# Optimization experiments

Hardware: AMD Instinct MI355X
Metric: run time of the kernel (lower is better)

The kernel has to match this reference:

```python
import jax, jax.numpy as jnp
import numpy as np

C, U, V, D, B = 5, 6144, 6144, 64, 4096  # classes, users, items, feat dim, batch pairs


def setup_inputs() -> dict:
    key = jax.random.key(0)
    ks = jax.random.split(key, 16)
    s = 1.0 / np.sqrt(D)
    adj = (jax.random.uniform(ks[0], (C, U, V)) < 0.01).astype(jnp.float32)
    return {
        "u": jax.random.randint(ks[1], (B,), 0, U),
        "v": jax.random.randint(ks[2], (B,), 0, V),
        "u_emb": jax.random.normal(ks[3], (U, D), jnp.float32) * 0.1,
        "v_emb": jax.random.normal(ks[4], (V, D), jnp.float32) * 0.1,
        "W1u": jax.random.normal(ks[5], (C, D, D), jnp.float32) * s,
        "b1u": jnp.zeros((C, D), jnp.float32),
        "W1v": jax.random.normal(ks[6], (C, D, D), jnp.float32) * s,
        "b1v": jnp.zeros((C, D), jnp.float32),
        "W2u": jax.random.normal(ks[7], (C, D, D), jnp.float32) * s,
        "b2u": jnp.zeros((C, D), jnp.float32),
        "W2v": jax.random.normal(ks[8], (C, D, D), jnp.float32) * s,
        "b2v": jnp.zeros((C, D), jnp.float32),
        "Q": jax.random.normal(ks[9], (C, D, D), jnp.float32) * s,
        "adj": adj,
    }


def reference(u, v, u_emb, v_emb, W1u, b1u, W1v, b1v, W2u, b2u, W2v, b2v, Q, adj):
    # ---- layer 1: per-class graph convolution, summed over rating classes ----
    # user codes aggregate item features through adj_c; item codes through adj_c^T
    msg_v = jnp.einsum("vd,cde->cve", v_emb, W1v)            # [C,V,D]
    h_u = jax.nn.relu(jnp.einsum("cuv,cve->ue", adj, msg_v) + b1v.sum(0))  # [U,D]
    msg_u = jnp.einsum("ud,cde->cue", u_emb, W1u)            # [C,U,D]
    h_v = jax.nn.relu(jnp.einsum("cuv,cue->ve", adj, msg_u) + b1u.sum(0))  # [V,D]
    # ---- layer 2 ----
    z_u = jnp.einsum("cuv,cve->ue", adj, jnp.einsum("vd,cde->cve", h_v, W2u)) + b2u.sum(0)
    z_v = jnp.einsum("cuv,cue->ve", adj, jnp.einsum("ud,cde->cue", h_u, W2v)) + b2v.sum(0)
    # ---- bilinear decoder over batch of (user, item) pairs ----
    zu = z_u[u]                                              # [B,D] gather
    zv = z_v[v]                                              # [B,D] gather
    logits = jnp.einsum("bd,cde,be->bc", zu, Q, zv)          # [B,C] per-class rating logits
    return logits
```

## Files before the change

kernel.cpp:

```cpp
#include <hip/hip_runtime.h>

#define NC   5
#define NU   6144
#define NV   6144
#define ND   64
#define NB   4096
#define CAP  128
#define NW   192

__device__ __forceinline__ unsigned int spread4(unsigned int x) {
  x &= 0xFFu;
  x = (x | (x << 12)) & 0x000F000Fu;
  x = (x | (x << 6))  & 0x03030303u;
  x = (x | (x << 3))  & 0x11111111u;
  return x;
}

__global__ __launch_bounds__(256) void k_bitmask(
    const float* __restrict__ adj,
    unsigned int* __restrict__ rowmask,
    unsigned int* __restrict__ colmask) {
  __shared__ unsigned int rowwords[64][8];
  const int b = blockIdx.x;
  const int c  = b / 2304;
  const int rem = b - c * 2304;
  const int tu = rem / 24;
  const int tv = rem - tu * 24;
  const int wave = threadIdx.x >> 6;
  const int lane = threadIdx.x & 63;

  for (int rr = 0; rr < 16; ++rr) {
    const int r = wave * 16 + rr;
    const float4* src = (const float4*)(adj +
        ((size_t)(c * NU + tu * 64 + r) * NV + tv * 256));
    const float4 a = src[lane];
    const unsigned long long b0 = __ballot(a.x != 0.0f);
    const unsigned long long b1 = __ballot(a.y != 0.0f);
    const unsigned long long b2 = __ballot(a.z != 0.0f);
    const unsigned long long b3 = __ballot(a.w != 0.0f);
    if (lane < 8) {
      const unsigned int e0 = spread4((unsigned int)(b0 >> (lane * 8)));
      const unsigned int e1 = spread4((unsigned int)(b1 >> (lane * 8)));
      const unsigned int e2 = spread4((unsigned int)(b2 >> (lane * 8)));
      const unsigned int e3 = spread4((unsigned int)(b3 >> (lane * 8)));
      rowwords[r][lane] = e0 | (e1 << 1) | (e2 << 2) | (e3 << 3);
    }
  }
  __syncthreads();

  {
    const int r2 = threadIdx.x >> 2;
    const int k  = threadIdx.x & 3;
    uint2 w;
    w.x = rowwords[r2][k * 2 + 0];
    w.y = rowwords[r2][k * 2 + 1];
    *(uint2*)(rowmask + (size_t)(c * NU + tu * 64 + r2) * NW + tv * 8 + k * 2) = w;
  }

  {
    const int j = threadIdx.x;
    const int w = j >> 5, bit = j & 31;
    unsigned int w0 = 0, w1 = 0;
    #pragma unroll
    for (int r = 0; r < 32; ++r) {
      w0 |= ((rowwords[r][w]      >> bit) & 1u) << r;
      w1 |= ((rowwords[r + 32][w] >> bit) & 1u) << r;
    }
    uint2 ww; ww.x = w0; ww.y = w1;
    *(uint2*)(colmask + (size_t)(c * NV + tv * 256 + j) * NW + tu * 2) = ww;
  }
}

__global__ __launch_bounds__(256) void k_expand(
    const unsigned int* __restrict__ mask,
    int* __restrict__ cnt,
    unsigned short* __restrict__ idx) {
  const int wave = threadIdx.x >> 6;
  const int lane = threadIdx.x & 63;
  const int R = blockIdx.x * 4 + wave;
  const unsigned int* mrow = mask + (size_t)R * NW;
  const unsigned int w0 = mrow[lane];
  const unsigned int w1 = mrow[lane + 64];
  const unsigned int w2 = mrow[lane + 128];
  const int t0 = __popc(w0), t1 = __popc(w1), t2 = __popc(w2);
  int p0 = t0, p1 = t1, p2 = t2;
  #pragma unroll
  for (int d = 1; d < 64; d <<= 1) {
    const int y0 = __shfl_up(p0, d, 64);
    const int y1 = __shfl_up(p1, d, 64);
    const int y2 = __shfl_up(p2, d, 64);
    if (lane >= d) { p0 += y0; p1 += y1; p2 += y2; }
  }
  const int T0 = __shfl(p0, 63, 64);
  const int T1 = __shfl(p1, 63, 64);
  const int T2 = __shfl(p2, 63, 64);
  if (lane == 0) cnt[R] = T0 + T1 + T2;
  unsigned short* orow = idx + (size_t)R * CAP;
  int e0 = p0 - t0;
  int e1 = T0 + p1 - t1;
  int e2 = T0 + T1 + p2 - t2;
  unsigned int m;
  m = w0;
  while (m) { int bb = __ffs(m) - 1; if (e0 < CAP) orow[e0] = (unsigned short)(lane * 32 + bb); ++e0; m &= m - 1; }
  m = w1;
  while (m) { int bb = __ffs(m) - 1; if (e1 < CAP) orow[e1] = (unsigned short)((lane + 64) * 32 + bb); ++e1; m &= m - 1; }
  m = w2;
  while (m) { int bb = __ffs(m) - 1; if (e2 < CAP) orow[e2] = (unsigned short)((lane + 128) * 32 + bb); ++e2; m &= m - 1; }
}

__global__ __launch_bounds__(256) void k_emb_transform(
    const float* __restrict__ emb,
    const float* __restrict__ W,
    float* __restrict__ out,
    int N) {
  const int c    = blockIdx.y;
  const int lane = threadIdx.x & 63;
  const int wave = threadIdx.x >> 6;
  const float* Wc = W + c * 64 * 64;
  float w[64];
  #pragma unroll
  for (int d = 0; d < 64; ++d) w[d] = Wc[d * 64 + lane];
  const int row0 = blockIdx.x * 64 + wave;
  for (int i = 0; i < 16; ++i) {
    const int r = row0 + i * 4;
    const float* er = emb + (size_t)r * 64;
    float acc = 0.0f;
    #pragma unroll
    for (int d = 0; d < 64; ++d) acc = fmaf(er[d], w[d], acc);
    out[((size_t)c * N + r) * 64 + lane] = acc;
  }
}

__global__ __launch_bounds__(256) void k_spmm(
    const int* __restrict__ cnt,
    const unsigned short* __restrict__ idx,
    const float* __restrict__ msg,
    const float* __restrict__ bias,
    float* __restrict__ out,
    int M, int N, int do_relu) {
  __shared__ float4 red4[4][16];
  const int r    = blockIdx.x;
  const int wave = threadIdx.x >> 6;
  const int lane = threadIdx.x & 63;
  const int g    = lane >> 4;
  const int e16  = lane & 15;
  float4 acc = make_float4(0.f, 0.f, 0.f, 0.f);
  for (int c = wave; c < NC; c += 4) {
    int n = cnt[c * M + r];
    n = n > CAP ? CAP : n;
    const unsigned short* l = idx + (size_t)(c * M + r) * CAP;
    const float4* msgc = (const float4*)msg + (size_t)c * N * 16;
    for (int i = 0; i < n; i += 4) {
      const int ig = i + g;
      if (ig < n) {
        const float4 x = msgc[(int)l[ig] * 16 + e16];
        acc.x += x.x; acc.y += x.y; acc.z += x.z; acc.w += x.w;
      }
    }
  }
  #pragma unroll
  for (int off = 16; off < 64; off <<= 1) {
    acc.x += __shfl_xor(acc.x, off, 64);
    acc.y += __shfl_xor(acc.y, off, 64);
    acc.z += __shfl_xor(acc.z, off, 64);
    acc.w += __shfl_xor(acc.w, off, 64);
  }
  if (lane < 16) red4[wave][e16] = acc;
  __syncthreads();
  if (threadIdx.x < 16) {
    const int e = threadIdx.x;
    float4 s = red4[0][e];
    #pragma unroll
    for (int w = 1; w < 4; ++w) {
      s.x += red4[w][e].x; s.y += red4[w][e].y;
      s.z += red4[w][e].z; s.w += red4[w][e].w;
    }
    #pragma unroll
    for (int c = 0; c < NC; ++c) {
      const float4 bb = ((const float4*)bias)[c * 16 + e];
      s.x += bb.x; s.y += bb.y; s.z += bb.z; s.w += bb.w;
    }
    if (do_relu) {
      s.x = fmaxf(s.x, 0.f); s.y = fmaxf(s.y, 0.f);
      s.z = fmaxf(s.z, 0.f); s.w = fmaxf(s.w, 0.f);
    }
    ((float4*)out)[(size_t)r * 16 + e] = s;
  }
}

__global__ __launch_bounds__(256) void k_decoder(
    const int* __restrict__ uu, const int* __restrict__ vv,
    const float* __restrict__ z_u, const float* __restrict__ z_v,
    const float* __restrict__ Q,
    float* __restrict__ out) {
  const int lane = threadIdx.x & 63;
  const int wave = threadIdx.x >> 6;
  const int b = blockIdx.x * 4 + wave;
  const int ub = uu[b];
  const int vb = vv[b];
  const float zve = z_v[(size_t)vb * 64 + lane];
  const float* zu = z_u + (size_t)ub * 64;
  #pragma unroll
  for (int c = 0; c < NC; ++c) {
    const float* Qc = Q + c * 64 * 64;
    float t = 0.0f;
    #pragma unroll
    for (int d = 0; d < 64; ++d) t = fmaf(zu[d], Qc[d * 64 + lane], t);
    float p = t * zve;
    #pragma unroll
    for (int off = 32; off > 0; off >>= 1) p += __shfl_xor(p, off, 64);
    if (lane == 0) out[(size_t)b * NC + c] = p;
  }
}

extern "C" void kernel_launch(void* const* d_in, const int* in_sizes, int n_in,
                              void* d_out, int out_size, void* d_ws, size_t ws_size,
                              hipStream_t stream) {
  const int*   u     = (const int*)d_in[0];
  const int*   v     = (const int*)d_in[1];
  const float* u_emb = (const float*)d_in[2];
  const float* v_emb = (const float*)d_in[3];
  const float* W1u   = (const float*)d_in[4];
  const float* b1u   = (const float*)d_in[5];
  const float* W1v   = (const float*)d_in[6];
  const float* b1v   = (const float*)d_in[7];
  const float* W2u   = (const float*)d_in[8];
  const float* b2u   = (const float*)d_in[9];
  const float* W2v   = (const float*)d_in[10];
  const float* b2v   = (const float*)d_in[11];
  const float* Q     = (const float*)d_in[12];
  const float* adj   = (const float*)d_in[13];
  float* out = (float*)d_out;

  char* ws = (char*)d_ws;
  int* csr_cnt = (int*)ws;
  int* csc_cnt = csr_cnt + NC * NU;
  unsigned short* csr_idx = (unsigned short*)(ws + 245760);
  unsigned short* csc_idx = (unsigned short*)(ws + 245760 + 7864320);
  char* maskbase = ws + 245760 + 2 * 7864320;
  unsigned int* rowmask = (unsigned int*)maskbase;
  unsigned int* colmask = (unsigned int*)(maskbase + 23592960);
  float* msgA = (float*)maskbase;
  float* msgB = (float*)(maskbase + 7864320);
  float* h_u  = (float*)(maskbase + 15728640);
  float* h_v  = (float*)(maskbase + 17301504);
  float* z_u  = (float*)(maskbase + 18874368);
  float* z_v  = (float*)(maskbase + 20447232);

  k_bitmask<<<5 * 96 * 24, 256, 0, stream>>>(adj, rowmask, colmask);
  k_expand<<<NC * NU / 4, 256, 0, stream>>>(rowmask, csr_cnt, csr_idx);
  k_expand<<<NC * NV / 4, 256, 0, stream>>>(colmask, csc_cnt, csc_idx);

  const dim3 gT(NU / 64, NC);
  k_emb_transform<<<gT, 256, 0, stream>>>(v_emb, W1v, msgA, NV);
  k_emb_transform<<<gT, 256, 0, stream>>>(u_emb, W1u, msgB, NU);
  k_spmm<<<NU, 256, 0, stream>>>(csr_cnt, csr_idx, msgA, b1v, h_u, NU, NV, 1);
  k_spmm<<<NV, 256, 0, stream>>>(csc_cnt, csc_idx, msgB, b1u, h_v, NV, NU, 1);
  k_emb_transform<<<gT, 256, 0, stream>>>(h_v, W2u, msgA, NV);
  k_emb_transform<<<gT, 256, 0, stream>>>(h_u, W2v, msgB, NU);
  k_spmm<<<NU, 256, 0, stream>>>(csr_cnt, csr_idx, msgA, b2u, z_u, NU, NV, 0);
  k_spmm<<<NV, 256, 0, stream>>>(csc_cnt, csc_idx, msgB, b2v, z_v, NV, NU, 0);
  k_decoder<<<NB / 4, 256, 0, stream>>>(u, v, z_u, z_v, Q, out);
}
```

Baseline: 1.388 ms.

## Reorder graph conv to aggregate-then-transform and batch adjacency loads in bitmask

The per-class graph convolution is reassociated: raw embeddings are gathered and summed per class through the CSR/CSC lists first, and the 64x64 weight transform is applied afterwards in a fused 5-class GEMM kernel that also adds the bias and ReLU. This removes the per-class message tables and lets the gather read a single compact embedding table that is more cache-friendly. The gather gets four independent accumulators for more loads in flight. The bitmask kernel now issues all 16 row loads before the ballots to raise memory-level parallelism. The cost is an extra aggregate buffer round-trip and a different floating-point summation order.

```diff
diff --git a/kernel.cpp b/kernel.cpp
--- a/kernel.cpp
+++ b/kernel.cpp
@@ -29,21 +29,26 @@
   const int wave = threadIdx.x >> 6;
   const int lane = threadIdx.x & 63;
 
+  float4 av[16];
+  {
+    const float* base = adj +
+        ((size_t)(c * NU + tu * 64 + wave * 16) * NV + tv * 256);
+    #pragma unroll
+    for (int rr = 0; rr < 16; ++rr)
+      av[rr] = ((const float4*)(base + (size_t)rr * NV))[lane];
+  }
+  #pragma unroll
   for (int rr = 0; rr < 16; ++rr) {
-    const int r = wave * 16 + rr;
-    const float4* src = (const float4*)(adj +
-        ((size_t)(c * NU + tu * 64 + r) * NV + tv * 256));
-    const float4 a = src[lane];
-    const unsigned long long b0 = __ballot(a.x != 0.0f);
-    const unsigned long long b1 = __ballot(a.y != 0.0f);
-    const unsigned long long b2 = __ballot(a.z != 0.0f);
-    const unsigned long long b3 = __ballot(a.w != 0.0f);
+    const unsigned long long b0 = __ballot(av[rr].x != 0.0f);
+    const unsigned long long b1 = __ballot(av[rr].y != 0.0f);
+    const unsigned long long b2 = __ballot(av[rr].z != 0.0f);
+    const unsigned long long b3 = __ballot(av[rr].w != 0.0f);
     if (lane < 8) {
       const unsigned int e0 = spread4((unsigned int)(b0 >> (lane * 8)));
       const unsigned int e1 = spread4((unsigned int)(b1 >> (lane * 8)));
       const unsigned int e2 = spread4((unsigned int)(b2 >> (lane * 8)));
       const unsigned int e3 = spread4((unsigned int)(b3 >> (lane * 8)));
-      rowwords[r][lane] = e0 | (e1 << 1) | (e2 << 2) | (e3 << 3);
+      rowwords[wave * 16 + rr][lane] = e0 | (e1 << 1) | (e2 << 2) | (e3 << 3);
     }
   }
   __syncthreads();
@@ -108,83 +113,93 @@
   while (m) { int bb = __ffs(m) - 1; if (e2 < CAP) orow[e2] = (unsigned short)((lane + 128) * 32 + bb); ++e2; m &= m - 1; }
 }
 
-__global__ __launch_bounds__(256) void k_emb_transform(
-    const float* __restrict__ emb,
-    const float* __restrict__ W,
-    float* __restrict__ out,
-    int N) {
-  const int c    = blockIdx.y;
-  const int lane = threadIdx.x & 63;
-  const int wave = threadIdx.x >> 6;
-  const float* Wc = W + c * 64 * 64;
-  float w[64];
-  #pragma unroll
-  for (int d = 0; d < 64; ++d) w[d] = Wc[d * 64 + lane];
-  const int row0 = blockIdx.x * 64 + wave;
-  for (int i = 0; i < 16; ++i) {
-    const int r = row0 + i * 4;
-    const float* er = emb + (size_t)r * 64;
-    float acc = 0.0f;
-    #pragma unroll
-    for (int d = 0; d < 64; ++d) acc = fmaf(er[d], w[d], acc);
-    out[((size_t)c * N + r) * 64 + lane] = acc;
-  }
-}
-
-__global__ __launch_bounds__(256) void k_spmm(
+__global__ __launch_bounds__(256) void k_gather(
     const int* __restrict__ cnt,
     const unsigned short* __restrict__ idx,
-    const float* __restrict__ msg,
+    const float* __restrict__ table,
+    float* __restrict__ agg) {
+  __shared__ float4 red4[4][16];
+  const int wave = threadIdx.x >> 6;
+  const int lane = threadIdx.x & 63;
+  const int R = blockIdx.x * 4 + wave;
+  const int g    = lane >> 4;
+  const int e16  = lane & 15;
+  int n = cnt[R];
+  n = n > CAP ? CAP : n;
+  const unsigned short* l = idx + (size_t)R * CAP;
+  const float4* tab = (const float4*)table;
+  float4 a0 = make_float4(0.f,0.f,0.f,0.f), a1 = a0, a2 = a0, a3 = a0;
+  int i = 0;
+  for (; i + 16 <= n; i += 16) {
+    const int j0 = l[i + g], j1 = l[i + 4 + g];
+    const int j2 = l[i + 8 + g], j3 = l[i + 12 + g];
+    const float4 x0 = tab[j0 * 16 + e16];
+    const float4 x1 = tab[j1 * 16 + e16];
+    const float4 x2 = tab[j2 * 16 + e16];
+    const float4 x3 = tab[j3 * 16 + e16];
+    a0.x += x0.x; a0.y += x0.y; a0.z += x0.z; a0.w += x0.w;
+    a1.x += x1.x; a1.y += x1.y; a1.z += x1.z; a1.w += x1.w;
+    a2.x += x2.x; a2.y += x2.y; a2.z += x2.z; a2.w += x2.w;
+    a3.x += x3.x; a3.y += x3.y; a3.z += x3.z; a3.w += x3.w;
+  }
+  for (; i + 4 <= n; i += 4) {
+    const float4 x = tab[(int)l[i + g] * 16 + e16];
+    a0.x += x.x; a0.y += x.y; a0.z += x.z; a0.w += x.w;
+  }
+  if (i + g < n) {
+    const float4 x = tab[(int)l[i + g] * 16 + e16];
+    a1.x += x.x; a1.y += x.y; a1.z += x.z; a1.w += x.w;
+  }
+  a0.x += a1.x + a2.x + a3.x;
+  a0.y += a1.y + a2.y + a3.y;
+  a0.z += a1.z + a2.z + a3.z;
+  a0.w += a1.w + a2.w + a3.w;
+  #pragma unroll
+  for (int off = 16; off < 64; off <<= 1) {
+    a0.x += __shfl_xor(a0.x, off, 64);
+    a0.y += __shfl_xor(a0.y, off, 64);
+    a0.z += __shfl_xor(a0.z, off, 64);
+    a0.w += __shfl_xor(a0.w, off, 64);
+  }
+  if (g == 0) red4[wave][e16] = a0;
+  __syncthreads();
+  if (g == 0) ((float4*)agg)[(size_t)R * 16 + e16] = red4[wave][e16];
+}
+
+__global__ __launch_bounds__(256) void k_gemm5(
+    const float* __restrict__ agg,
+    const float* __restrict__ W,
     const float* __restrict__ bias,
     float* __restrict__ out,
-    int M, int N, int do_relu) {
-  __shared__ float4 red4[4][16];
-  const int r    = blockIdx.x;
-  const int wave = threadIdx.x >> 6;
-  const int lane = threadIdx.x & 63;
-  const int g    = lane >> 4;
-  const int e16  = lane & 15;
-  float4 acc = make_float4(0.f, 0.f, 0.f, 0.f);
-  for (int c = wave; c < NC; c += 4) {
-    int n = cnt[c * M + r];
-    n = n > CAP ? CAP : n;
-    const unsigned short* l = idx + (size_t)(c * M + r) * CAP;
-    const float4* msgc = (const float4*)msg + (size_t)c * N * 16;
-    for (int i = 0; i < n; i += 4) {
-      const int ig = i + g;
-      if (ig < n) {
-        const float4 x = msgc[(int)l[ig] * 16 + e16];
-        acc.x += x.x; acc.y += x.y; acc.z += x.z; acc.w += x.w;
+    int M, int do_relu) {
+  const int lane = threadIdx.x & 63;
+  const int wave = threadIdx.x >> 6;
+  const int r0 = blockIdx.x * 16 + wave * 4;
+  float bs = 0.0f;
+  #pragma unroll
+  for (int c = 0; c < NC; ++c) bs += bias[c * 64 + lane];
+  float acc[4] = {bs, bs, bs, bs};
+  for (int c = 0; c < NC; ++c) {
+    float w[64];
+    #pragma unroll
+    for (int d = 0; d < 64; ++d) w[d] = W[c * 4096 + d * 64 + lane];
+    #pragma unroll
+    for (int r = 0; r < 4; ++r) {
+      const float4* ar = (const float4*)(agg + ((size_t)c * M + r0 + r) * 64);
+      #pragma unroll
+      for (int d4 = 0; d4 < 16; ++d4) {
+        const float4 a = ar[d4];
+        acc[r] = fmaf(a.x, w[d4 * 4 + 0], acc[r]);
+        acc[r] = fmaf(a.y, w[d4 * 4 + 1], acc[r]);
+        acc[r] = fmaf(a.z, w[d4 * 4 + 2], acc[r]);
+        acc[r] = fmaf(a.w, w[d4 * 4 + 3], acc[r]);
       }
     }
   }
   #pragma unroll
-  for (int off = 16; off < 64; off <<= 1) {
-    acc.x += __shfl_xor(acc.x, off, 64);
-    acc.y += __shfl_xor(acc.y, off, 64);
-    acc.z += __shfl_xor(acc.z, off, 64);
-    acc.w += __shfl_xor(acc.w, off, 64);
-  }
-  if (lane < 16) red4[wave][e16] = acc;
-  __syncthreads();
-  if (threadIdx.x < 16) {
-    const int e = threadIdx.x;
-    float4 s = red4[0][e];
-    #pragma unroll
-    for (int w = 1; w < 4; ++w) {
-      s.x += red4[w][e].x; s.y += red4[w][e].y;
-      s.z += red4[w][e].z; s.w += red4[w][e].w;
-    }
-    #pragma unroll
-    for (int c = 0; c < NC; ++c) {
-      const float4 bb = ((const float4*)bias)[c * 16 + e];
-      s.x += bb.x; s.y += bb.y; s.z += bb.z; s.w += bb.w;
-    }
-    if (do_relu) {
-      s.x = fmaxf(s.x, 0.f); s.y = fmaxf(s.y, 0.f);
-      s.z = fmaxf(s.z, 0.f); s.w = fmaxf(s.w, 0.f);
-    }
-    ((float4*)out)[(size_t)r * 16 + e] = s;
+  for (int r = 0; r < 4; ++r) {
+    const float x = do_relu ? fmaxf(acc[r], 0.0f) : acc[r];
+    out[(size_t)(r0 + r) * 64 + lane] = x;
   }
 }
 
@@ -240,8 +255,8 @@
   char* maskbase = ws + 245760 + 2 * 7864320;
   unsigned int* rowmask = (unsigned int*)maskbase;
   unsigned int* colmask = (unsigned int*)(maskbase + 23592960);
-  float* msgA = (float*)maskbase;
-  float* msgB = (float*)(maskbase + 7864320);
+  float* aggA = (float*)maskbase;
+  float* aggB = (float*)(maskbase + 7864320);
   float* h_u  = (float*)(maskbase + 15728640);
   float* h_v  = (float*)(maskbase + 17301504);
   float* z_u  = (float*)(maskbase + 18874368);
@@ -251,14 +266,13 @@
   k_expand<<<NC * NU / 4, 256, 0, stream>>>(rowmask, csr_cnt, csr_idx);
   k_expand<<<NC * NV / 4, 256, 0, stream>>>(colmask, csc_cnt, csc_idx);
 
-  const dim3 gT(NU / 64, NC);
-  k_emb_transform<<<gT, 256, 0, stream>>>(v_emb, W1v, msgA, NV);
-  k_emb_transform<<<gT, 256, 0, stream>>>(u_emb, W1u, msgB, NU);
-  k_spmm<<<NU, 256, 0, stream>>>(csr_cnt, csr_idx, msgA, b1v, h_u, NU, NV, 1);
-  k_spmm<<<NV, 256, 0, stream>>>(csc_cnt, csc_idx, msgB, b1u, h_v, NV, NU, 1);
-  k_emb_transform<<<gT, 256, 0, stream>>>(h_v, W2u, msgA, NV);
-  k_emb_transform<<<gT, 256, 0, stream>>>(h_u, W2v, msgB, NU);
-  k_spmm<<<NU, 256, 0, stream>>>(csr_cnt, csr_idx, msgA, b2u, z_u, NU, NV, 0);
-  k_spmm<<<NV, 256, 0, stream>>>(csc_cnt, csc_idx, msgB, b2v, z_v, NV, NU, 0);
+  k_gather<<<NC * NU / 4, 256, 0, stream>>>(csr_cnt, csr_idx, v_emb, aggA);
+  k_gather<<<NC * NV / 4, 256, 0, stream>>>(csc_cnt, csc_idx, u_emb, aggB);
+  k_gemm5<<<NU / 16, 256, 0, stream>>>(aggA, W1v, b1v, h_u, NU, 1);
+  k_gemm5<<<NV / 16, 256, 0, stream>>>(aggB, W1u, b1u, h_v, NV, 1);
+  k_gather<<<NC * NU / 4, 256, 0, stream>>>(csr_cnt, csr_idx, h_v, aggA);
+  k_gather<<<NC * NV / 4, 256, 0, stream>>>(csc_cnt, csc_idx, h_u, aggB);
+  k_gemm5<<<NU / 16, 256, 0, stream>>>(aggA, W2u, b2u, z_u, NU, 0);
+  k_gemm5<<<NV / 16, 256, 0, stream>>>(aggB, W2v, b2v, z_v, NV, 0);
   k_decoder<<<NB / 4, 256, 0, stream>>>(u, v, z_u, z_v, Q, out);
 }
```

Measured after the change: 1.263 ms. 1.1x faster.
